# Kernel tuning notes

Measured on AMD Instinct MI355X. Metric: run time of the kernel, lower is better.

The kernel has to match this reference:

```python
import jax, jax.numpy as jnp
from jax import lax
import numpy as np

SAMPLE_RATIO = 0.25
K = 20          # nsample from group_args
SLOPE = 0.2     # leakyrelu negative_slope
EPS = 1e-5      # BatchNorm eps


def fps(p, m):
    """Furthest point sampling. p: [B,N,3] -> idx [B,m] int32."""
    B, N, _ = p.shape

    def step(carry, _):
        dist, last_idx = carry                      # [B,N], [B]
        last_pt = jnp.take_along_axis(p, last_idx[:, None, None], axis=1)  # [B,1,3]
        d = jnp.sum((p - last_pt) ** 2, axis=-1)    # [B,N]
        dist = jnp.minimum(dist, d)
        nxt = jnp.argmax(dist, axis=1).astype(jnp.int32)
        return (dist, nxt), last_idx

    dist0 = jnp.full((B, N), 1e10, dtype=p.dtype)
    idx0 = jnp.zeros((B,), dtype=jnp.int32)
    _, idxs = lax.scan(step, (dist0, idx0), None, length=m)
    return jnp.transpose(idxs)                      # [B,m]


def knn_idx(q, p, k):
    """q: [B,M,3] queries, p: [B,N,3] -> [B,M,k] indices of k nearest."""
    # squared distances, [B,M,N] (the memory-bound intermediate)
    d = (jnp.sum(q * q, -1)[:, :, None]
         + jnp.sum(p * p, -1)[:, None, :]
         - 2.0 * jnp.einsum('bmd,bnd->bmn', q, p))
    _, idx = lax.top_k(-d, k)
    return idx


def convblock(x, W, g, b):
    """1x1 Conv2d (bias=False) -> leakyrelu(0.2) -> BatchNorm2d (train-mode)."""
    x = jnp.einsum('oc,bcmk->bomk', W, x)
    x = jnp.where(x >= 0, x, SLOPE * x)
    mean = jnp.mean(x, axis=(0, 2, 3), keepdims=True)
    var = jnp.var(x, axis=(0, 2, 3), keepdims=True)
    return g[None, :, None, None] * (x - mean) * lax.rsqrt(var + EPS) + b[None, :, None, None]


def setup_inputs() -> dict:
    key = jax.random.key(0)
    ks = jax.random.split(key, 4)
    C = 64
    p = jax.random.normal(ks[0], (4, 8192, 3), dtype=jnp.float32)
    # kaiming-normal-ish conv weights (1x1 kernels flattened to [out,in])
    W1 = jax.random.normal(ks[1], (C, 6), dtype=jnp.float32) * np.sqrt(2.0 / 6)
    W2 = jax.random.normal(ks[2], (C, C), dtype=jnp.float32) * np.sqrt(2.0 / C)
    W3 = jax.random.normal(ks[3], (C, C), dtype=jnp.float32) * np.sqrt(2.0 / C)
    ones = jnp.ones((C,), jnp.float32)
    zeros = jnp.zeros((C,), jnp.float32)
    return {"p": p, "W1": W1, "g1": ones, "b1": zeros,
            "W2": W2, "g2": ones, "b2": zeros,
            "W3": W3, "g3": ones, "b3": zeros}


def reference(p, W1, g1, b1, W2, g2, b2, W3, g3, b3):
    B, N, _ = p.shape
    M = int(N * SAMPLE_RATIO)
    # features default to xyz: f = p^T, [B,3,N]; we keep [B,N,3] layout for gathers
    idx = fps(p, M)                                              # [B,M]
    p1 = jnp.take_along_axis(p, idx[:, :, None], axis=1)         # [B,M,3]
    nidx = knn_idx(p1, p, K)                                     # [B,M,K]
    batch = jnp.arange(B)[:, None, None]
    grouped = p[batch, nidx]                                     # [B,M,K,3] gathered xyz (== gathered features)
    dp = grouped - p1[:, :, None, :]                             # [B,M,K,3] relative coords
    # cat((dp, gf), dim=1) in channel-first layout -> [B,6,M,K]
    gf = jnp.concatenate([dp, grouped], axis=-1)                 # [B,M,K,6]
    x = jnp.transpose(gf, (0, 3, 1, 2))                          # [B,6,M,K]
    x = convblock(x, W1, g1, b1)
    x = convblock(x, W2, g2, b2)
    x = convblock(x, W3, g3, b3)
    return jnp.max(x, axis=-1)                                   # [B,64,M]
```

## Files before the change

### kernel.cpp

```cpp
#include <hip/hip_runtime.h>
#include <cstdint>
#include <cstddef>


#define B_ 4
#define N_ 8192
#define M_ 2048
#define K_ 20
#define BMK (B_*M_*K_)
#define EPS_ 1e-5f
#define TILE_ 1024
#define PERS 248

typedef unsigned long long ull;
typedef float f32x2 __attribute__((ext_vector_type(2)));

__device__ __forceinline__ ull packkey(float d, int idx) {
  unsigned int bb = __float_as_uint(d);
  bb ^= (bb & 0x80000000u) ? 0xFFFFFFFFu : 0x80000000u;
  return ((ull)bb << 32) | (unsigned int)idx;
}
__device__ __forceinline__ float keymaxf(ull k) {
  unsigned int hb = (unsigned int)(k >> 32);
  unsigned int fb = (hb & 0x80000000u) ? (hb ^ 0x80000000u) : ~hb;
  return __uint_as_float(fb);
}
__device__ __forceinline__ void insert20(ull* keys, ull key) {
#pragma unroll
  for (int i = 19; i > 0; --i) {
    ull lo = keys[i-1];
    keys[i] = (key < lo) ? lo : ((key < keys[i]) ? key : keys[i]);
  }
  keys[0] = (key < keys[0]) ? key : keys[0];
}

#define DPPMAXU(V, CTRL) {                                                           \
    unsigned int nh = (unsigned int)__builtin_amdgcn_update_dpp(                     \
        (int)V, (int)V, CTRL, 0xF, 0xF, false);                                      \
    V = (nh > V) ? nh : V; }

__global__ __launch_bounds__(512)
void fpsknn_kernel(const float* __restrict__ p, float* __restrict__ p1,
                   float* __restrict__ gfp, const float* __restrict__ W1,
                   float* __restrict__ stats, int* __restrict__ prog) {
  __shared__ union {
    struct { float4 pts4[N_]; unsigned int slotsv[2][8]; int idxsel[2]; } f;
    struct { float4 tile[TILE_]; ull mk[8*32*20]; float bs[128]; } k;
  } sm;
  const int tid = threadIdx.x;

  if (blockIdx.x < B_) {
#pragma clang fp contract(off)
    const int b = blockIdx.x;
    const float* pb = p + (size_t)b * (N_*3);
    float* p1b = p1 + (size_t)b * (M_*3);
    float4* pts4 = sm.f.pts4;
    const int wv = tid >> 6;
    const int base = tid * 16;
    f32x2 X[8], Y[8], Z[8], D[8];
#pragma unroll
    for (int j = 0; j < 8; ++j) {
      int i = base + 2*j;
      float x0 = pb[i*3+0], y0 = pb[i*3+1], z0 = pb[i*3+2];
      float x1 = pb[i*3+3], y1 = pb[i*3+4], z1 = pb[i*3+5];
      X[j] = (f32x2){x0, x1};
      Y[j] = (f32x2){y0, y1};
      Z[j] = (f32x2){z0, z1};
      D[j] = (f32x2){1e10f, 1e10f};
      pts4[i]   = make_float4(x0, y0, z0, 0.f);
      pts4[i+1] = make_float4(x1, y1, z1, 0.f);
    }
    if (tid < 2) sm.f.idxsel[tid] = 0x7FFFFFFF;
    float qx = pb[0], qy = pb[1], qz = pb[2];
    if (tid == 0) { p1b[0] = qx; p1b[1] = qy; p1b[2] = qz; }
    __syncthreads();
    for (int t = 1; t < M_; ++t) {
      const int cur = t & 1;
      f32x2 q2x = (f32x2){qx, qx};
      f32x2 q2y = (f32x2){qy, qy};
      f32x2 q2z = (f32x2){qz, qz};
      f32x2 tmx = (f32x2){-1.f, -1.f};
#pragma unroll
      for (int j = 0; j < 8; ++j) {
        f32x2 dx = X[j] - q2x;
        f32x2 dy = Y[j] - q2y;
        f32x2 dz = Z[j] - q2z;
        f32x2 s = (dx*dx + dy*dy) + dz*dz;
        f32x2 dj = __builtin_elementwise_min(D[j], s);
        D[j] = dj;
        tmx = __builtin_elementwise_max(tmx, dj);
      }
      float tm = fmaxf(tmx.x, tmx.y);
      const unsigned int tmb = __float_as_uint(tm);
      unsigned int hv = tmb;
      DPPMAXU(hv, 0x111)
      DPPMAXU(hv, 0x112)
      DPPMAXU(hv, 0x114)
      DPPMAXU(hv, 0x118)
      DPPMAXU(hv, 0x142)
      DPPMAXU(hv, 0x143)
      if ((tid & 63) == 63) sm.f.slotsv[cur][wv] = hv;
      __syncthreads();
      if (tid == 0) sm.f.idxsel[cur ^ 1] = 0x7FFFFFFF;
      unsigned int g = sm.f.slotsv[cur][0];
#pragma unroll
      for (int j = 1; j < 8; ++j) { unsigned int s2 = sm.f.slotsv[cur][j]; g = (s2 > g) ? s2 : g; }
      if (tmb == g) {
        int fj = 0x7FFFFFFF;
#pragma unroll
        for (int j = 7; j >= 0; --j) {
          if (__float_as_uint(D[j].y) == g) fj = base + 2*j + 1;
          if (__float_as_uint(D[j].x) == g) fj = base + 2*j;
        }
        atomicMin(&sm.f.idxsel[cur], fj);
      }
      __syncthreads();
      int sel = sm.f.idxsel[cur];
      sel = __builtin_amdgcn_readfirstlane(sel);
      float4 qv = pts4[sel];
      qx = qv.x; qy = qv.y; qz = qv.z;
      if (tid == 0) {
        p1b[t*3+0] = qx; p1b[t*3+1] = qy; p1b[t*3+2] = qz;
        if ((t & 63) == 63)
          __hip_atomic_store(&prog[b], t, __ATOMIC_RELEASE, __HIP_MEMORY_SCOPE_AGENT);
      }
    }
    if (tid == 0)
      __hip_atomic_store(&prog[b], M_, __ATOMIC_RELEASE, __HIP_MEMORY_SCOPE_AGENT);
    return;
  }

  float4* tile = sm.k.tile;
  ull* mk = sm.k.mk;
  float* gfl = (float*)sm.k.tile;
  float* bs = sm.k.bs;
  for (int ord = (int)blockIdx.x - B_; ord < 1024; ord += PERS) {
    const int b = ord & 3;
    const int q0 = (ord >> 2) * 8;
    if (tid == 0) {
      while (__hip_atomic_load(&prog[b], __ATOMIC_ACQUIRE, __HIP_MEMORY_SCOPE_AGENT) < q0 + 7)
        __builtin_amdgcn_s_sleep(16);
    }
    __syncthreads();
    { int pv = __hip_atomic_load(&prog[b], __ATOMIC_ACQUIRE, __HIP_MEMORY_SCOPE_AGENT);
      asm volatile("" :: "v"(pv)); }

    const int ql = (tid >> 5) & 7;
    const int part = tid & 31;
    const int m = q0 + ql;
    const float* pb = p + (size_t)b*(N_*3);
    const float* qp_ = p1 + ((size_t)b*M_ + m)*3;
    float qx = qp_[0], qy = qp_[1], qz = qp_[2];
    float qq = __fadd_rn(__fadd_rn(__fmul_rn(qx,qx), __fmul_rn(qy,qy)), __fmul_rn(qz,qz));
    ull keys[20];
#pragma unroll
    for (int i = 0; i < 20; ++i) keys[i] = 0xFF8000007FFFFFFFull;
    float maxf = __uint_as_float(0x7F800000u);
    for (int t0 = 0; t0 < N_; t0 += TILE_) {
      __syncthreads();
      for (int i = tid; i < TILE_; i += 512) {
        float x = pb[(t0+i)*3+0], y = pb[(t0+i)*3+1], z = pb[(t0+i)*3+2];
        float pp = __fadd_rn(__fadd_rn(__fmul_rn(x,x), __fmul_rn(y,y)), __fmul_rn(z,z));
        tile[i] = make_float4(x, y, z, pp);
      }
      __syncthreads();
      if (tid < 256) {
        const int sbase = part * 32;
        for (int s = 0; s < 32; ++s) {
          int ss = sbase + ((s + part) & 31);
          float4 pt = tile[ss];
          float qp = fmaf(pt.z, qz, fmaf(pt.y, qy, __fmul_rn(pt.x, qx)));
          float d = __fsub_rn(__fadd_rn(qq, pt.w), __fmul_rn(2.0f, qp));
          if (d <= maxf) {
            ull key = packkey(d, t0 + ss);
            if (key < keys[19]) { insert20(keys, key); maxf = keymaxf(keys[19]); }
          }
        }
      }
    }
    if (tid < 256) {
      ull* myslot = &mk[(ql*32 + part)*20];
#pragma unroll
      for (int i = 0; i < 20; ++i) myslot[i] = keys[i];
    }
    __syncthreads();
    if (tid < 256 && part == 0) {
      for (int pp2 = 1; pp2 < 32; ++pp2) {
        const ull* os = &mk[(ql*32 + pp2)*20];
        for (int i = 0; i < 20; ++i) {
          ull k = os[i];
          if (k >= keys[19]) break;
          insert20(keys, k);
        }
      }
      ull* myslot = &mk[(ql*32)*20];
#pragma unroll
      for (int i = 0; i < 20; ++i) myslot[i] = keys[i];
    }
    __syncthreads();
    for (int w = tid; w < 8*K_; w += 512) {
      int ql2 = w / K_;
      int kk = w - ql2*K_;
      ull key = mk[ql2*32*20 + kk];
      int idx = (int)(unsigned int)(key & 0xFFFFFFFFu);
      float gx = pb[idx*3+0], gy = pb[idx*3+1], gz = pb[idx*3+2];
      int m2 = q0 + ql2;
      const float* qv = p1 + ((size_t)b*M_ + m2)*3;
      size_t col = ((size_t)(b*M_ + m2))*K_ + kk;
      float d0 = __fsub_rn(gx, qv[0]);
      float d1 = __fsub_rn(gy, qv[1]);
      float d2 = __fsub_rn(gz, qv[2]);
      gfp[0*BMK + col] = d0;
      gfp[1*BMK + col] = d1;
      gfp[2*BMK + col] = d2;
      gfp[3*BMK + col] = gx;
      gfp[4*BMK + col] = gy;
      gfp[5*BMK + col] = gz;
      gfl[w*6+0] = d0; gfl[w*6+1] = d1; gfl[w*6+2] = d2;
      gfl[w*6+3] = gx; gfl[w*6+4] = gy; gfl[w*6+5] = gz;
    }
    __syncthreads();
    {
      const int lane = tid & 63;
      const int grp = tid >> 6;
      float w1r[6];
#pragma unroll
      for (int c = 0; c < 6; ++c) w1r[c] = W1[lane*6 + c];
      float acc = 0.f, accq = 0.f;
      for (int cc = 0; cc < 20; ++cc) {
        const float* gv = &gfl[(grp*20 + cc)*6];
        float y = __fmul_rn(w1r[0], gv[0]);
#pragma unroll
        for (int c = 1; c < 6; ++c) y = fmaf(w1r[c], gv[c], y);
        float u = (y >= 0.f) ? y : 0.2f*y;
        acc += u;
        accq = fmaf(u, u, accq);
      }
      if (tid < 128) bs[tid] = 0.f;
      __syncthreads();
      atomicAdd(&bs[lane], acc);
      atomicAdd(&bs[64+lane], accq);
      __syncthreads();
      if (tid < 128) atomicAdd(&stats[tid], bs[tid]);
    }
  }
}

__device__ __forceinline__ void bn_coeff(const float* __restrict__ st,
                                         const float* __restrict__ g,
                                         const float* __restrict__ bb,
                                         int o, float& A, float& C) {
  const float inv = 1.0f / (float)BMK;
  float mean = st[o] * inv;
  float var  = st[64+o] * inv - mean*mean;
  float a = g[o] / sqrtf(var + EPS_);
  A = a;
  C = fmaf(-a, mean, bb[o]);
}

__device__ __forceinline__ void gridbar(int* c, int expected) {
  __syncthreads();
  if (threadIdx.x == 0) {
    __hip_atomic_fetch_add(c, 1, __ATOMIC_ACQ_REL, __HIP_MEMORY_SCOPE_AGENT);
    while (__hip_atomic_load(c, __ATOMIC_ACQUIRE, __HIP_MEMORY_SCOPE_AGENT) < expected)
      __builtin_amdgcn_s_sleep(2);
  }
  __syncthreads();
}

__global__ __launch_bounds__(256)
void tail_kernel(const float* __restrict__ gfp, const float* __restrict__ W1,
                 float* __restrict__ stats,
                 const float* __restrict__ g1, const float* __restrict__ b1,
                 const float* __restrict__ W2, float* __restrict__ u2t,
                 const float* __restrict__ W3,
                 const float* __restrict__ g2, const float* __restrict__ b2,
                 const float* __restrict__ g3, const float* __restrict__ b3,
                 float* __restrict__ out, int* __restrict__ bar) {
  const int tid = threadIdx.x;
  const int nthr = (int)gridDim.x * 256;
  const int nblk = (int)gridDim.x;
  __shared__ float sA[64], sC[64];
  __shared__ float bs[128];

  if (tid < 64) bn_coeff(stats, g1, b1, tid, sA[tid], sC[tid]);
  __syncthreads();
  for (int col = (int)blockIdx.x*256 + tid; col < BMK; col += nthr) {
    float gf[6];
#pragma unroll
    for (int c = 0; c < 6; ++c) gf[c] = gfp[c*BMK + col];
    float x1[64];
#pragma unroll
    for (int c = 0; c < 64; ++c) {
      float y = __fmul_rn(W1[c*6+0], gf[0]);
#pragma unroll
      for (int i = 1; i < 6; ++i) y = fmaf(W1[c*6+i], gf[i], y);
      float u = (y >= 0.f) ? y : 0.2f*y;
      x1[c] = fmaf(sA[c], u, sC[c]);
    }
    float* ob = u2t + (size_t)col * 64;
    for (int o4 = 0; o4 < 16; ++o4) {
      float y0 = 0.f, y1 = 0.f, y2 = 0.f, y3 = 0.f;
#pragma unroll
      for (int c = 0; c < 64; ++c) {
        float xc = x1[c];
        y0 = fmaf(W2[(o4*4+0)*64+c], xc, y0);
        y1 = fmaf(W2[(o4*4+1)*64+c], xc, y1);
        y2 = fmaf(W2[(o4*4+2)*64+c], xc, y2);
        y3 = fmaf(W2[(o4*4+3)*64+c], xc, y3);
      }
      float4 v;
      v.x = (y0 >= 0.f) ? y0 : 0.2f*y0;
      v.y = (y1 >= 0.f) ? y1 : 0.2f*y1;
      v.z = (y2 >= 0.f) ? y2 : 0.2f*y2;
      v.w = (y3 >= 0.f) ? y3 : 0.2f*y3;
      ((float4*)ob)[o4] = v;
    }
  }
  gridbar(&bar[0], nblk);

  {
    const float4* u4 = (const float4*)u2t;
    const int nf4 = BMK * 16;
    float a0=0,a1=0,a2=0,a3=0,s0=0,s1=0,s2=0,s3=0;
    for (int i = (int)blockIdx.x*256 + tid; i < nf4; i += nthr) {
      float4 v = u4[i];
      a0 += v.x; s0 = fmaf(v.x, v.x, s0);
      a1 += v.y; s1 = fmaf(v.y, v.y, s1);
      a2 += v.z; s2 = fmaf(v.z, v.z, s2);
      a3 += v.w; s3 = fmaf(v.w, v.w, s3);
    }
    const int c0 = (4*tid) & 63;
    if (tid < 128) bs[tid] = 0.f;
    __syncthreads();
    atomicAdd(&bs[c0+0], a0); atomicAdd(&bs[c0+1], a1);
    atomicAdd(&bs[c0+2], a2); atomicAdd(&bs[c0+3], a3);
    atomicAdd(&bs[64+c0+0], s0); atomicAdd(&bs[64+c0+1], s1);
    atomicAdd(&bs[64+c0+2], s2); atomicAdd(&bs[64+c0+3], s3);
    __syncthreads();
    if (tid < 128) atomicAdd(&stats[128 + tid], bs[tid]);
  }
  gridbar(&bar[1], nblk);

  const int lane = tid & 63;
  float w[64];
  float bb = 0.f;
  {
    if (tid < 64) bn_coeff(stats + 128, g2, b2, tid, sA[tid], sC[tid]);
    __syncthreads();
#pragma unroll
    for (int c = 0; c < 64; ++c) w[c] = W3[lane*64 + c] * sA[c];
#pragma unroll
    for (int c = 0; c < 64; ++c) bb = fmaf(W3[lane*64 + c], sC[c], bb);
    const int gw = ((int)blockIdx.x*256 + tid) >> 6;
    const int nw = nthr >> 6;
    float acc = 0.f, accq = 0.f;
    for (int col = gw; col < BMK; col += nw) {
      const float4* u4 = (const float4*)(u2t + (size_t)col*64);
      float y = bb;
#pragma unroll
      for (int c4 = 0; c4 < 16; ++c4) {
        float4 v = u4[c4];
        y = fmaf(w[4*c4+0], v.x, y);
        y = fmaf(w[4*c4+1], v.y, y);
        y = fmaf(w[4*c4+2], v.z, y);
        y = fmaf(w[4*c4+3], v.w, y);
      }
      float u = (y >= 0.f) ? y : 0.2f*y;
      acc += u; accq = fmaf(u, u, accq);
    }
    if (tid < 128) bs[tid] = 0.f;
    __syncthreads();
    atomicAdd(&bs[lane], acc);
    atomicAdd(&bs[64+lane], accq);
    __syncthreads();
    if (tid < 128) atomicAdd(&stats[256 + tid], bs[tid]);
  }
  gridbar(&bar[2], nblk);

  {
    float A3, C3;
    bn_coeff(stats + 256, g3, b3, lane, A3, C3);
    const int w0 = ((int)blockIdx.x*256 + tid) >> 6;
    const int nw = nthr >> 6;
    for (int wv = w0; wv < B_*M_; wv += nw) {
      float mx = -3.4e38f, mn = 3.4e38f;
      for (int k = 0; k < K_; ++k) {
        const float4* u4 = (const float4*)(u2t + ((size_t)wv*K_ + k)*64);
        float y = bb;
#pragma unroll
        for (int c4 = 0; c4 < 16; ++c4) {
          float4 v = u4[c4];
          y = fmaf(w[4*c4+0], v.x, y);
          y = fmaf(w[4*c4+1], v.y, y);
          y = fmaf(w[4*c4+2], v.z, y);
          y = fmaf(w[4*c4+3], v.w, y);
        }
        float u = (y >= 0.f) ? y : 0.2f*y;
        mx = fmaxf(mx, u); mn = fminf(mn, u);
      }
      float r = (A3 >= 0.f) ? mx : mn;
      int b = wv >> 11, m = wv & 2047;
      out[((size_t)(b*64 + lane))*M_ + m] = fmaf(A3, r, C3);
    }
  }
}

extern "C" void kernel_launch(void* const* d_in, const int* in_sizes, int n_in,
                              void* d_out, int out_size, void* d_ws, size_t ws_size,
                              hipStream_t stream) {
  const float* p  = (const float*)d_in[0];
  const float* W1 = (const float*)d_in[1];
  const float* g1 = (const float*)d_in[2];
  const float* b1 = (const float*)d_in[3];
  const float* W2 = (const float*)d_in[4];
  const float* g2 = (const float*)d_in[5];
  const float* b2 = (const float*)d_in[6];
  const float* W3 = (const float*)d_in[7];
  const float* g3 = (const float*)d_in[8];
  const float* b3 = (const float*)d_in[9];
  float* out = (float*)d_out;
  char* ws = (char*)d_ws;

  float* p1    = (float*)(ws);
  float* gfp   = (float*)(ws + 131072);
  float* u2t   = (float*)(ws + 4194304);
  float* stats = (float*)(ws + 46137344);
  int*   prog  = (int*)(ws + 46138880);
  int*   bar   = (int*)(ws + 46138896);

  hipMemsetAsync((void*)stats, 0, 1568, stream);
  hipLaunchKernelGGL(fpsknn_kernel, dim3(B_ + PERS), dim3(512), 0, stream,
                     p, p1, gfp, W1, stats, prog);
  hipLaunchKernelGGL(tail_kernel,   dim3(256), dim3(256), 0, stream,
                     gfp, W1, stats, g1, b1, W2, u2t, W3, g2, b2, g3, b3, out, bar);
}
```

Before: 2.514 ms.

## Fuse BN statistics into conv passes and cache per-group max/min in tail kernel

The tail kernel now runs conv2 with one wave per column and one output channel per lane, staging the conv1 result through LDS. It accumulates the BN2 statistics while writing u2t, which removes the separate statistics pass over u2t. The conv3 pass computes the BN3 statistics and the per-group max/min together and stores them to scratch, so the final phase only applies the affine transform. This drops one grid barrier and one full conv3 recompute over the large u2t buffer. The grid doubles to 512 blocks, which relies on all blocks being co-resident for the software grid barrier, and the max/min scratch reuses workspace that earlier held p1 and gfp.

```diff
diff --git a/kernel.cpp b/kernel.cpp
--- a/kernel.cpp
+++ b/kernel.cpp
@@ -276,114 +276,84 @@
                  const float* __restrict__ W3,
                  const float* __restrict__ g2, const float* __restrict__ b2,
                  const float* __restrict__ g3, const float* __restrict__ b3,
-                 float* __restrict__ out, int* __restrict__ bar) {
+                 float* __restrict__ out, int* __restrict__ bar,
+                 float* __restrict__ pmx, float* __restrict__ pmn) {
   const int tid = threadIdx.x;
-  const int nthr = (int)gridDim.x * 256;
   const int nblk = (int)gridDim.x;
+  const int lane = tid & 63;
+  const int wid = ((int)blockIdx.x*256 + tid) >> 6;
+  const int nw = (nblk*256) >> 6;
   __shared__ float sA[64], sC[64];
   __shared__ float bs[128];
-
-  if (tid < 64) bn_coeff(stats, g1, b1, tid, sA[tid], sC[tid]);
-  __syncthreads();
-  for (int col = (int)blockIdx.x*256 + tid; col < BMK; col += nthr) {
-    float gf[6];
-#pragma unroll
-    for (int c = 0; c < 6; ++c) gf[c] = gfp[c*BMK + col];
-    float x1[64];
-#pragma unroll
-    for (int c = 0; c < 64; ++c) {
-      float y = __fmul_rn(W1[c*6+0], gf[0]);
-#pragma unroll
-      for (int i = 1; i < 6; ++i) y = fmaf(W1[c*6+i], gf[i], y);
+  __shared__ float xbuf[4][64];
+  float* xb = xbuf[(tid >> 6) & 3];
+
+  {
+    if (tid < 64) bn_coeff(stats, g1, b1, tid, sA[tid], sC[tid]);
+    __syncthreads();
+    float w1r[6];
+#pragma unroll
+    for (int c = 0; c < 6; ++c) w1r[c] = W1[lane*6 + c];
+    const float sAl = sA[lane], sCl = sC[lane];
+    float wrow[64];
+#pragma unroll
+    for (int c = 0; c < 64; ++c) wrow[c] = W2[lane*64 + c];
+    float acc = 0.f, accq = 0.f;
+    float gfn[6];
+    int col = wid;
+    if (col < BMK) {
+#pragma unroll
+      for (int c = 0; c < 6; ++c) gfn[c] = gfp[c*BMK + col];
+    }
+    for (; col < BMK; col += nw) {
+      float gfc[6];
+#pragma unroll
+      for (int c = 0; c < 6; ++c) gfc[c] = gfn[c];
+      if (col + nw < BMK) {
+#pragma unroll
+        for (int c = 0; c < 6; ++c) gfn[c] = gfp[c*BMK + (col + nw)];
+      }
+      float y = __fmul_rn(w1r[0], gfc[0]);
+#pragma unroll
+      for (int c = 1; c < 6; ++c) y = fmaf(w1r[c], gfc[c], y);
       float u = (y >= 0.f) ? y : 0.2f*y;
-      x1[c] = fmaf(sA[c], u, sC[c]);
-    }
-    float* ob = u2t + (size_t)col * 64;
-    for (int o4 = 0; o4 < 16; ++o4) {
-      float y0 = 0.f, y1 = 0.f, y2 = 0.f, y3 = 0.f;
-#pragma unroll
-      for (int c = 0; c < 64; ++c) {
-        float xc = x1[c];
-        y0 = fmaf(W2[(o4*4+0)*64+c], xc, y0);
-        y1 = fmaf(W2[(o4*4+1)*64+c], xc, y1);
-        y2 = fmaf(W2[(o4*4+2)*64+c], xc, y2);
-        y3 = fmaf(W2[(o4*4+3)*64+c], xc, y3);
-      }
-      float4 v;
-      v.x = (y0 >= 0.f) ? y0 : 0.2f*y0;
-      v.y = (y1 >= 0.f) ? y1 : 0.2f*y1;
-      v.z = (y2 >= 0.f) ? y2 : 0.2f*y2;
-      v.w = (y3 >= 0.f) ? y3 : 0.2f*y3;
-      ((float4*)ob)[o4] = v;
-    }
+      float x1v = fmaf(sAl, u, sCl);
+      xb[lane] = x1v;
+      float yo = 0.f;
+      const float4* xb4 = (const float4*)xb;
+#pragma unroll
+      for (int c4 = 0; c4 < 16; ++c4) {
+        float4 v = xb4[c4];
+        yo = fmaf(wrow[4*c4+0], v.x, yo);
+        yo = fmaf(wrow[4*c4+1], v.y, yo);
+        yo = fmaf(wrow[4*c4+2], v.z, yo);
+        yo = fmaf(wrow[4*c4+3], v.w, yo);
+      }
+      float u2 = (yo >= 0.f) ? yo : 0.2f*yo;
+      u2t[(size_t)col*64 + lane] = u2;
+      acc += u2;
+      accq = fmaf(u2, u2, accq);
+    }
+    if (tid < 128) bs[tid] = 0.f;
+    __syncthreads();
+    atomicAdd(&bs[lane], acc);
+    atomicAdd(&bs[64+lane], accq);
+    __syncthreads();
+    if (tid < 128) atomicAdd(&stats[128 + tid], bs[tid]);
   }
   gridbar(&bar[0], nblk);
 
-  {
-    const float4* u4 = (const float4*)u2t;
-    const int nf4 = BMK * 16;
-    float a0=0,a1=0,a2=0,a3=0,s0=0,s1=0,s2=0,s3=0;
-    for (int i = (int)blockIdx.x*256 + tid; i < nf4; i += nthr) {
-      float4 v = u4[i];
-      a0 += v.x; s0 = fmaf(v.x, v.x, s0);
-      a1 += v.y; s1 = fmaf(v.y, v.y, s1);
-      a2 += v.z; s2 = fmaf(v.z, v.z, s2);
-      a3 += v.w; s3 = fmaf(v.w, v.w, s3);
-    }
-    const int c0 = (4*tid) & 63;
-    if (tid < 128) bs[tid] = 0.f;
-    __syncthreads();
-    atomicAdd(&bs[c0+0], a0); atomicAdd(&bs[c0+1], a1);
-    atomicAdd(&bs[c0+2], a2); atomicAdd(&bs[c0+3], a3);
-    atomicAdd(&bs[64+c0+0], s0); atomicAdd(&bs[64+c0+1], s1);
-    atomicAdd(&bs[64+c0+2], s2); atomicAdd(&bs[64+c0+3], s3);
-    __syncthreads();
-    if (tid < 128) atomicAdd(&stats[128 + tid], bs[tid]);
-  }
-  gridbar(&bar[1], nblk);
-
-  const int lane = tid & 63;
-  float w[64];
+  float w3[64];
   float bb = 0.f;
   {
     if (tid < 64) bn_coeff(stats + 128, g2, b2, tid, sA[tid], sC[tid]);
     __syncthreads();
 #pragma unroll
-    for (int c = 0; c < 64; ++c) w[c] = W3[lane*64 + c] * sA[c];
+    for (int c = 0; c < 64; ++c) w3[c] = W3[lane*64 + c] * sA[c];
 #pragma unroll
     for (int c = 0; c < 64; ++c) bb = fmaf(W3[lane*64 + c], sC[c], bb);
-    const int gw = ((int)blockIdx.x*256 + tid) >> 6;
-    const int nw = nthr >> 6;
     float acc = 0.f, accq = 0.f;
-    for (int col = gw; col < BMK; col += nw) {
-      const float4* u4 = (const float4*)(u2t + (size_t)col*64);
-      float y = bb;
-#pragma unroll
-      for (int c4 = 0; c4 < 16; ++c4) {
-        float4 v = u4[c4];
-        y = fmaf(w[4*c4+0], v.x, y);
-        y = fmaf(w[4*c4+1], v.y, y);
-        y = fmaf(w[4*c4+2], v.z, y);
-        y = fmaf(w[4*c4+3], v.w, y);
-      }
-      float u = (y >= 0.f) ? y : 0.2f*y;
-      acc += u; accq = fmaf(u, u, accq);
-    }
-    if (tid < 128) bs[tid] = 0.f;
-    __syncthreads();
-    atomicAdd(&bs[lane], acc);
-    atomicAdd(&bs[64+lane], accq);
-    __syncthreads();
-    if (tid < 128) atomicAdd(&stats[256 + tid], bs[tid]);
-  }
-  gridbar(&bar[2], nblk);
-
-  {
-    float A3, C3;
-    bn_coeff(stats + 256, g3, b3, lane, A3, C3);
-    const int w0 = ((int)blockIdx.x*256 + tid) >> 6;
-    const int nw = nthr >> 6;
-    for (int wv = w0; wv < B_*M_; wv += nw) {
+    for (int wv = wid; wv < B_*M_; wv += nw) {
       float mx = -3.4e38f, mn = 3.4e38f;
       for (int k = 0; k < K_; ++k) {
         const float4* u4 = (const float4*)(u2t + ((size_t)wv*K_ + k)*64);
@@ -391,14 +361,33 @@
 #pragma unroll
         for (int c4 = 0; c4 < 16; ++c4) {
           float4 v = u4[c4];
-          y = fmaf(w[4*c4+0], v.x, y);
-          y = fmaf(w[4*c4+1], v.y, y);
-          y = fmaf(w[4*c4+2], v.z, y);
-          y = fmaf(w[4*c4+3], v.w, y);
+          y = fmaf(w3[4*c4+0], v.x, y);
+          y = fmaf(w3[4*c4+1], v.y, y);
+          y = fmaf(w3[4*c4+2], v.z, y);
+          y = fmaf(w3[4*c4+3], v.w, y);
         }
         float u = (y >= 0.f) ? y : 0.2f*y;
+        acc += u; accq = fmaf(u, u, accq);
         mx = fmaxf(mx, u); mn = fminf(mn, u);
       }
+      pmx[(size_t)wv*64 + lane] = mx;
+      pmn[(size_t)wv*64 + lane] = mn;
+    }
+    if (tid < 128) bs[tid] = 0.f;
+    __syncthreads();
+    atomicAdd(&bs[lane], acc);
+    atomicAdd(&bs[64+lane], accq);
+    __syncthreads();
+    if (tid < 128) atomicAdd(&stats[256 + tid], bs[tid]);
+  }
+  gridbar(&bar[1], nblk);
+
+  {
+    float A3, C3;
+    bn_coeff(stats + 256, g3, b3, lane, A3, C3);
+    for (int wv = wid; wv < B_*M_; wv += nw) {
+      float mx = pmx[(size_t)wv*64 + lane];
+      float mn = pmn[(size_t)wv*64 + lane];
       float r = (A3 >= 0.f) ? mx : mn;
       int b = wv >> 11, m = wv & 2047;
       out[((size_t)(b*64 + lane))*M_ + m] = fmaf(A3, r, C3);
@@ -428,10 +417,13 @@
   float* stats = (float*)(ws + 46137344);
   int*   prog  = (int*)(ws + 46138880);
   int*   bar   = (int*)(ws + 46138896);
+  float* pmx   = (float*)(ws);
+  float* pmn   = (float*)(ws + 2097152);
 
   hipMemsetAsync((void*)stats, 0, 1568, stream);
   hipLaunchKernelGGL(fpsknn_kernel, dim3(B_ + PERS), dim3(512), 0, stream,
                      p, p1, gfp, W1, stats, prog);
-  hipLaunchKernelGGL(tail_kernel,   dim3(256), dim3(256), 0, stream,
-                     gfp, W1, stats, g1, b1, W2, u2t, W3, g2, b2, g3, b3, out, bar);
-}
+  hipLaunchKernelGGL(tail_kernel,   dim3(512), dim3(256), 0, stream,
+                     gfp, W1, stats, g1, b1, W2, u2t, W3, g2, b2, g3, b3, out, bar,
+                     pmx, pmn);
+}
```

Result: faster. 2.393 ms (-4.8%).
